# Kernel optimization log

Hardware: AMD Instinct MI355X
Metric: run time of the kernel (lower is better)

## Reference

```python
import jax, jax.numpy as jnp
import numpy as np
from jax import lax

NEG_INF = -jnp.inf

def _conv_same(x, w, b):
    # x: [B,C,H,W], w: [O,C,5,5], padding=2 (SAME for k=5)
    y = lax.conv_general_dilated(x, w, (1, 1), [(2, 2), (2, 2)],
                                 dimension_numbers=('NCHW', 'OIHW', 'NCHW'))
    return y + b[None, :, None, None]

def _maxpool3(x):
    # kernel=3, stride=3, VALID: 28x28 -> 9x9
    return lax.reduce_window(x, -jnp.inf, lax.max, (1, 1, 3, 3), (1, 1, 3, 3), 'VALID')

def _trunk(x, w1, b1, w2, b2):
    # x: [B,1,28,28] -> [B, 16*9*9]
    h = jax.nn.relu(_conv_same(x, w1, b1))
    h = jax.nn.relu(_conv_same(h, w2, b2))
    h = _maxpool3(h)
    return h.reshape(h.shape[0], -1)

def _iterator(state, c_w1, c_b1, c_w2, c_b2, c_wl, c_bl):
    # state: [B,28,28]
    B = state.shape[0]
    xd = state[:, None]                                   # [B,1,28,28]
    feat = _trunk(xd, c_w1, c_b1, c_w2, c_b2)             # [B,1296]
    w = jnp.tanh(feat @ c_wl + c_bl).reshape(B, 1, 13, 13)  # per-sample kernels [O=B,I=1,13,13]
    xp = jnp.pad(xd, ((0, 0), (0, 0), (6, 6), (6, 6)), constant_values=-1.0)  # [B,1,40,40]
    xg = xp.reshape(1, B, 40, 40)
    yg = lax.conv_general_dilated(xg, w, (1, 1), 'VALID',
                                  feature_group_count=B,
                                  dimension_numbers=('NCHW', 'OIHW', 'NCHW'))  # [1,B,28,28]
    return yg.reshape(B, 28, 28)

def setup_inputs() -> dict:
    key = jax.random.key(0)
    ks = jax.random.split(key, 13)
    s = 0.05
    B = 1024
    inp = {
        'x': jax.random.normal(ks[0], (B, 28, 28), jnp.float32),
        # determine_n params
        'n_w1': jax.random.normal(ks[1], (8, 1, 5, 5), jnp.float32) * s,
        'n_b1': jnp.zeros((8,), jnp.float32),
        'n_w2': jax.random.normal(ks[2], (16, 8, 5, 5), jnp.float32) * s,
        'n_b2': jnp.zeros((16,), jnp.float32),
        'n_wl': jax.random.normal(ks[3], (16 * 9 * 9, 10), jnp.float32) * s,
        'n_bl': jnp.zeros((10,), jnp.float32),
        # determine_conv params
        'c_w1': jax.random.normal(ks[4], (8, 1, 5, 5), jnp.float32) * s,
        'c_b1': jnp.zeros((8,), jnp.float32),
        'c_w2': jax.random.normal(ks[5], (16, 8, 5, 5), jnp.float32) * s,
        'c_b2': jnp.zeros((16,), jnp.float32),
        'c_wl': jax.random.normal(ks[6], (16 * 9 * 9, 13 * 13), jnp.float32) * s,
        'c_bl': jnp.zeros((13 * 13,), jnp.float32),
    }
    return inp

def reference(x, n_w1, n_b1, n_w2, n_b2, n_wl, n_bl,
              c_w1, c_b1, c_w2, c_b2, c_wl, c_bl):
    B = x.shape[0]
    xd = x.reshape(B, 1, 28, 28)
    # determine_n: soft natural number over {0..9}
    num = jnp.tanh(_trunk(xd, n_w1, n_b1, n_w2, n_b2) @ n_wl + n_bl)  # [B,10]
    # TmIter: weighted sum of iterates r_0..r_9, r_{k+1} = iterator(r_k)
    r = x
    out = num[:, 0, None, None] * r
    for k in range(1, 10):  # fixed 9-step unroll (num encodes naturals 0..9)
        r = _iterator(r, c_w1, c_b1, c_w2, c_b2, c_wl, c_bl)
        out = out + num[:, k, None, None] * r
    return out.reshape(-1, 28, 28)
```

## Files before the change

### kernel.cpp

```cpp
#include <hip/hip_runtime.h>
#include <math.h>

#define RP40S 44
#define H1W   31

struct SharedBufs {
    float rp40[2][40*RP40S];
    float h1p[8*28*H1W];
    float pbuf[1296];
    float wker[169];
    float num_s[10];
    int   next;
};

template<int OUT>
__device__ __forceinline__ void fc_tanh(const float* __restrict__ Wg,
                                        const float* __restrict__ bg,
                                        const float* __restrict__ p,
                                        float* __restrict__ dst, int tid)
{
    if (tid < OUT) {
        float a[8];
        #pragma unroll
        for (int u = 0; u < 8; ++u) a[u] = 0.f;
        #pragma unroll 4
        for (int i0 = 0; i0 < 1296; i0 += 8) {
            const float4 p0 = *(const float4*)&p[i0];
            const float4 p1 = *(const float4*)&p[i0+4];
            a[0] = fmaf(p0.x, Wg[(i0+0)*OUT + tid], a[0]);
            a[1] = fmaf(p0.y, Wg[(i0+1)*OUT + tid], a[1]);
            a[2] = fmaf(p0.z, Wg[(i0+2)*OUT + tid], a[2]);
            a[3] = fmaf(p0.w, Wg[(i0+3)*OUT + tid], a[3]);
            a[4] = fmaf(p1.x, Wg[(i0+4)*OUT + tid], a[4]);
            a[5] = fmaf(p1.y, Wg[(i0+5)*OUT + tid], a[5]);
            a[6] = fmaf(p1.z, Wg[(i0+6)*OUT + tid], a[6]);
            a[7] = fmaf(p1.w, Wg[(i0+7)*OUT + tid], a[7]);
        }
        float s = ((a[0]+a[1])+(a[2]+a[3])) + ((a[4]+a[5])+(a[6]+a[7])) + bg[tid];
        dst[tid] = tanhf(s);
    }
}

#define C2_LOADROW(dst, YY) {                                                  \
    int rr_ = crow0 + (YY); rr_ = rr_ < 2 ? 2 : (rr_ > 29 ? 29 : rr_);         \
    const float* hp_ = plane + (rr_ - 2)*H1W;                                  \
    _Pragma("unroll") for (int j = 0; j < 13; ++j) dst[j] = hp_[j]; }

#define C2_FMAROW(src, YY)                                                     \
    if ((unsigned)(crow0 + (YY) - 2) <= 27u) {                                 \
      _Pragma("unroll") for (int t = 0; t < 3; ++t) {                          \
        const int ky_ = (YY) - t;                                              \
        if (ky_ >= 0 && ky_ <= 4) {                                            \
          _Pragma("unroll") for (int kx = 0; kx < 5; ++kx) {                   \
            const float w_ = wreg[ky_*5+kx];                                   \
            _Pragma("unroll") for (int u = 0; u < 9; ++u)                      \
              acc[t*9+u] = fmaf(w_, src[u+kx], acc[t*9+u]); } } } }

__device__ __forceinline__ void trunk_pass(SharedBufs& sb,
                                           const float* __restrict__ rpc,
                                           int tid,
                                           const float* __restrict__ w1g,
                                           const float* __restrict__ b1g,
                                           const float* __restrict__ w2g,
                                           const float* __restrict__ b2g)
{
    if (tid < 224) {
        const int c = tid & 7;
        const int y = tid >> 3;
        float wreg[25];
        #pragma unroll
        for (int t = 0; t < 25; ++t) wreg[t] = w1g[c*25 + t];
        float csR[5];
        float S_all = 0.f, SR = 0.f;
        #pragma unroll
        for (int kx = 0; kx < 5; ++kx) {
            float a = wreg[kx] + wreg[5+kx] + wreg[10+kx] + wreg[15+kx] + wreg[20+kx];
            float ex = 0.f;
            if (y == 0)       ex = wreg[kx] + wreg[5+kx];
            else if (y == 1)  ex = wreg[kx];
            if (y == 26)      ex += wreg[20+kx];
            else if (y == 27) ex += wreg[15+kx] + wreg[20+kx];
            csR[kx] = a - ex;
            S_all += a; SR += csR[kx];
        }
        const float corrI = S_all - SR;
        const float bias  = b1g[c];
        float acc[28];
        #pragma unroll
        for (int x = 0; x < 28; ++x) acc[x] = bias + corrI;
        acc[0]  += csR[0] + csR[1];
        acc[1]  += csR[0];
        acc[26] += csR[4];
        acc[27] += csR[3] + csR[4];
        #pragma unroll
        for (int ky = 0; ky < 5; ++ky) {
            const float4* rr = (const float4*)&rpc[(y+4+ky)*RP40S + 4];
            float rv[32];
            #pragma unroll
            for (int q = 0; q < 8; ++q) {
                float4 t = rr[q];
                rv[q*4+0]=t.x; rv[q*4+1]=t.y; rv[q*4+2]=t.z; rv[q*4+3]=t.w;
            }
            #pragma unroll
            for (int kx = 0; kx < 5; ++kx) {
                const float w = wreg[ky*5+kx];
                #pragma unroll
                for (int x = 0; x < 28; ++x) acc[x] = fmaf(w, rv[x+kx], acc[x]);
            }
        }
        float* hp = &sb.h1p[(c*28 + y)*H1W + 2];
        #pragma unroll
        for (int x = 0; x < 28; ++x) hp[x] = fmaxf(acc[x], 0.f);
    }
    __syncthreads();

    if (tid < 240) {
        const int c    = tid / 15;
        const int rem  = tid % 15;
        const int pyg  = rem / 3;
        const int pxg  = rem % 3;
        const int col0 = pxg * 9;
        const float bias = b2g[c];
        #pragma unroll 1
        for (int h = 0; h < 2; ++h) {
            const int py = pyg*2 + h;
            if (py >= 9) break;
            const int crow0 = py * 3;
            float acc[27];
            #pragma unroll
            for (int i = 0; i < 27; ++i) acc[i] = bias;
            for (int ic = 0; ic < 8; ++ic) {
                float wreg[25];
                const float* wsrc = &w2g[(c*8+ic)*25];
                #pragma unroll
                for (int t = 0; t < 25; ++t) wreg[t] = wsrc[t];
                const float* plane = &sb.h1p[ic*28*H1W + col0];
                float ra[13], rb[13];
                C2_LOADROW(ra, 0)
                C2_LOADROW(rb, 1)  C2_FMAROW(ra, 0)
                C2_LOADROW(ra, 2)  C2_FMAROW(rb, 1)
                C2_LOADROW(rb, 3)  C2_FMAROW(ra, 2)
                C2_LOADROW(ra, 4)  C2_FMAROW(rb, 3)
                C2_LOADROW(rb, 5)  C2_FMAROW(ra, 4)
                C2_LOADROW(ra, 6)  C2_FMAROW(rb, 5)
                                   C2_FMAROW(ra, 6)
            }
            #pragma unroll
            for (int pxi = 0; pxi < 3; ++pxi) {
                float m = acc[pxi*3];
                #pragma unroll
                for (int dy = 0; dy < 3; ++dy)
                    #pragma unroll
                    for (int dx = 0; dx < 3; ++dx)
                        m = fmaxf(m, acc[dy*9 + pxi*3 + dx]);
                sb.pbuf[c*81 + py*9 + pxg*3 + pxi] = fmaxf(m, 0.f);
            }
        }
    }
    __syncthreads();
}

__device__ __forceinline__ void depthwise13_regs(SharedBufs& sb,
                                                 const float* __restrict__ rpc,
                                                 int y, int x0,
                                                 float& a0, float& a1,
                                                 float& a2, float& a3)
{
    a0=0.f; a1=0.f; a2=0.f; a3=0.f;
    #pragma unroll 1
    for (int ky = 0; ky < 13; ++ky) {
        const float4* rr = (const float4*)&rpc[(y+ky)*RP40S + x0];
        float rv[16];
        #pragma unroll
        for (int q = 0; q < 4; ++q) {
            float4 t = rr[q];
            rv[q*4+0]=t.x; rv[q*4+1]=t.y; rv[q*4+2]=t.z; rv[q*4+3]=t.w;
        }
        const float* wr = &sb.wker[ky*13];
        #pragma unroll
        for (int kx = 0; kx < 13; ++kx) {
            const float w = wr[kx];
            a0 = fmaf(w, rv[kx+0], a0);
            a1 = fmaf(w, rv[kx+1], a1);
            a2 = fmaf(w, rv[kx+2], a2);
            a3 = fmaf(w, rv[kx+3], a3);
        }
    }
}

__global__ __launch_bounds__(256) __attribute__((amdgpu_num_vgpr(168)))
void modeld_fused(const float* __restrict__ x,
                  const float* __restrict__ n_w1, const float* __restrict__ n_b1,
                  const float* __restrict__ n_w2, const float* __restrict__ n_b2,
                  const float* __restrict__ n_wl, const float* __restrict__ n_bl,
                  const float* __restrict__ c_w1, const float* __restrict__ c_b1,
                  const float* __restrict__ c_w2, const float* __restrict__ c_b2,
                  const float* __restrict__ c_wl, const float* __restrict__ c_bl,
                  float* __restrict__ out,
                  int* __restrict__ counter, int B)
{
    __shared__ SharedBufs sb;
    const int tid = threadIdx.x;
    const int dy  = tid / 7;
    const int dx0 = (tid % 7) * 4;

    for (int i = tid; i < 2*40*RP40S; i += 256) sb.rp40[0][i] = -1.f;
    for (int i = tid; i < 8*28*H1W;   i += 256) sb.h1p[i]  = 0.f;

    while (true) {
        if (tid == 0) sb.next = atomicAdd(counter, 1);
        __syncthreads();
        const int b = sb.next;
        if (b >= B) break;

        float cur[4] = {0.f, 0.f, 0.f, 0.f};
        if (tid < 196) {
            const float4 t = *(const float4*)&x[b*784 + dy*28 + dx0];
            cur[0]=t.x; cur[1]=t.y; cur[2]=t.z; cur[3]=t.w;
            float* rp = &sb.rp40[0][(dy+6)*RP40S + dx0 + 6];
            rp[0]=t.x; rp[1]=t.y; rp[2]=t.z; rp[3]=t.w;
        }
        __syncthreads();

        trunk_pass(sb, sb.rp40[0], tid, n_w1, n_b1, n_w2, n_b2);
        fc_tanh<10>(n_wl, n_bl, sb.pbuf, sb.num_s, tid);
        __syncthreads();

        float o[4];
        {
            const float n0 = sb.num_s[0];
            #pragma unroll
            for (int q = 0; q < 4; ++q) o[q] = n0 * cur[q];
        }

        int curbuf = 0;
        for (int k = 1; k <= 9; ++k) {
            const float* rpc = sb.rp40[curbuf];
            float*       rpn = sb.rp40[curbuf ^ 1];
            trunk_pass(sb, rpc, tid, c_w1, c_b1, c_w2, c_b2);
            fc_tanh<169>(c_wl, c_bl, sb.pbuf, sb.wker, tid);
            __syncthreads();
            if (tid < 196) {
                float a0, a1, a2, a3;
                depthwise13_regs(sb, rpc, dy, dx0, a0, a1, a2, a3);
                const float nk = sb.num_s[k];
                o[0] = fmaf(nk, a0, o[0]);
                o[1] = fmaf(nk, a1, o[1]);
                o[2] = fmaf(nk, a2, o[2]);
                o[3] = fmaf(nk, a3, o[3]);
                float* rp = &rpn[(dy+6)*RP40S + dx0 + 6];
                rp[0]=a0; rp[1]=a1; rp[2]=a2; rp[3]=a3;
            }
            __syncthreads();
            curbuf ^= 1;
        }

        if (tid < 196)
            *(float4*)&out[b*784 + dy*28 + dx0] = make_float4(o[0], o[1], o[2], o[3]);
    }
}

extern "C" void kernel_launch(void* const* d_in, const int* in_sizes, int n_in,
                              void* d_out, int out_size, void* d_ws, size_t ws_size,
                              hipStream_t stream)
{
    const float* x    = (const float*)d_in[0];
    const float* n_w1 = (const float*)d_in[1];
    const float* n_b1 = (const float*)d_in[2];
    const float* n_w2 = (const float*)d_in[3];
    const float* n_b2 = (const float*)d_in[4];
    const float* n_wl = (const float*)d_in[5];
    const float* n_bl = (const float*)d_in[6];
    const float* c_w1 = (const float*)d_in[7];
    const float* c_b1 = (const float*)d_in[8];
    const float* c_w2 = (const float*)d_in[9];
    const float* c_b2 = (const float*)d_in[10];
    const float* c_wl = (const float*)d_in[11];
    const float* c_bl = (const float*)d_in[12];
    float* out = (float*)d_out;

    const int B = in_sizes[0] / 784;
    hipMemsetAsync(d_ws, 0, sizeof(int), stream);
    const int grid = B < 768 ? B : 768;
    hipLaunchKernelGGL(modeld_fused, dim3(grid), dim3(256), 0, stream,
                       x, n_w1, n_b1, n_w2, n_b2, n_wl, n_bl,
                       c_w1, c_b1, c_w2, c_b2, c_wl, c_bl, out,
                       (int*)d_ws, B);
}
```

Before: 1.335 ms.

## Hoist conv1 border corrections, pad depthwise kernel rows, unroll FC deeper

Computes the conv1 bias and border-correction terms once per thread at kernel start instead of on every trunk pass, passing them in as scalars. Pads the 13x13 dynamic kernel rows to stride 16 so the depthwise loop can read weights with float4 LDS loads. Raises the FC loop unroll from 4 to 8. Keeping ten extra live scalars across the persistent loop adds register pressure under the fixed 168-VGPR cap, which could cause spills.

New measurement: 1.302 ms, median of 2. 1.03x faster.

```diff
diff --git a/kernel.cpp b/kernel.cpp
--- a/kernel.cpp
+++ b/kernel.cpp
@@ -8,12 +8,12 @@
     float rp40[2][40*RP40S];
     float h1p[8*28*H1W];
     float pbuf[1296];
-    float wker[169];
+    float wker[13*16];
     float num_s[10];
     int   next;
 };
 
-template<int OUT>
+template<int OUT, bool PAD>
 __device__ __forceinline__ void fc_tanh(const float* __restrict__ Wg,
                                         const float* __restrict__ bg,
                                         const float* __restrict__ p,
@@ -23,7 +23,7 @@
         float a[8];
         #pragma unroll
         for (int u = 0; u < 8; ++u) a[u] = 0.f;
-        #pragma unroll 4
+        #pragma unroll 8
         for (int i0 = 0; i0 < 1296; i0 += 8) {
             const float4 p0 = *(const float4*)&p[i0];
             const float4 p1 = *(const float4*)&p[i0+4];
@@ -37,8 +37,37 @@
             a[7] = fmaf(p1.w, Wg[(i0+7)*OUT + tid], a[7]);
         }
         float s = ((a[0]+a[1])+(a[2]+a[3])) + ((a[4]+a[5])+(a[6]+a[7])) + bg[tid];
-        dst[tid] = tanhf(s);
-    }
+        dst[PAD ? (tid/13)*16 + (tid%13) : tid] = tanhf(s);
+    }
+}
+
+__device__ __forceinline__ void conv1_corr(const float* __restrict__ w1g,
+                                           const float* __restrict__ b1g,
+                                           int c, int y,
+                                           float& base, float& e0, float& e1,
+                                           float& e26, float& e27)
+{
+    float wreg[25];
+    #pragma unroll
+    for (int t = 0; t < 25; ++t) wreg[t] = w1g[c*25 + t];
+    float csR[5];
+    float S_all = 0.f, SR = 0.f;
+    #pragma unroll
+    for (int kx = 0; kx < 5; ++kx) {
+        float a = wreg[kx] + wreg[5+kx] + wreg[10+kx] + wreg[15+kx] + wreg[20+kx];
+        float ex = 0.f;
+        if (y == 0)       ex = wreg[kx] + wreg[5+kx];
+        else if (y == 1)  ex = wreg[kx];
+        if (y == 26)      ex += wreg[20+kx];
+        else if (y == 27) ex += wreg[15+kx] + wreg[20+kx];
+        csR[kx] = a - ex;
+        S_all += a; SR += csR[kx];
+    }
+    base = b1g[c] + (S_all - SR);
+    e0  = csR[0] + csR[1];
+    e1  = csR[0];
+    e26 = csR[4];
+    e27 = csR[3] + csR[4];
 }
 
 #define C2_LOADROW(dst, YY) {                                                  \
@@ -60,9 +89,10 @@
                                            const float* __restrict__ rpc,
                                            int tid,
                                            const float* __restrict__ w1g,
-                                           const float* __restrict__ b1g,
                                            const float* __restrict__ w2g,
-                                           const float* __restrict__ b2g)
+                                           const float* __restrict__ b2g,
+                                           float base, float e0, float e1,
+                                           float e26, float e27)
 {
     if (tid < 224) {
         const int c = tid & 7;
@@ -70,28 +100,13 @@
         float wreg[25];
         #pragma unroll
         for (int t = 0; t < 25; ++t) wreg[t] = w1g[c*25 + t];
-        float csR[5];
-        float S_all = 0.f, SR = 0.f;
-        #pragma unroll
-        for (int kx = 0; kx < 5; ++kx) {
-            float a = wreg[kx] + wreg[5+kx] + wreg[10+kx] + wreg[15+kx] + wreg[20+kx];
-            float ex = 0.f;
-            if (y == 0)       ex = wreg[kx] + wreg[5+kx];
-            else if (y == 1)  ex = wreg[kx];
-            if (y == 26)      ex += wreg[20+kx];
-            else if (y == 27) ex += wreg[15+kx] + wreg[20+kx];
-            csR[kx] = a - ex;
-            S_all += a; SR += csR[kx];
-        }
-        const float corrI = S_all - SR;
-        const float bias  = b1g[c];
         float acc[28];
         #pragma unroll
-        for (int x = 0; x < 28; ++x) acc[x] = bias + corrI;
-        acc[0]  += csR[0] + csR[1];
-        acc[1]  += csR[0];
-        acc[26] += csR[4];
-        acc[27] += csR[3] + csR[4];
+        for (int x = 0; x < 28; ++x) acc[x] = base;
+        acc[0]  += e0;
+        acc[1]  += e1;
+        acc[26] += e26;
+        acc[27] += e27;
         #pragma unroll
         for (int ky = 0; ky < 5; ++ky) {
             const float4* rr = (const float4*)&rpc[(y+4+ky)*RP40S + 4];
@@ -176,10 +191,16 @@
             float4 t = rr[q];
             rv[q*4+0]=t.x; rv[q*4+1]=t.y; rv[q*4+2]=t.z; rv[q*4+3]=t.w;
         }
-        const float* wr = &sb.wker[ky*13];
+        const float4* wq = (const float4*)&sb.wker[ky*16];
+        float wv[16];
+        #pragma unroll
+        for (int q = 0; q < 4; ++q) {
+            float4 t = wq[q];
+            wv[q*4+0]=t.x; wv[q*4+1]=t.y; wv[q*4+2]=t.z; wv[q*4+3]=t.w;
+        }
         #pragma unroll
         for (int kx = 0; kx < 13; ++kx) {
-            const float w = wr[kx];
+            const float w = wv[kx];
             a0 = fmaf(w, rv[kx+0], a0);
             a1 = fmaf(w, rv[kx+1], a1);
             a2 = fmaf(w, rv[kx+2], a2);
@@ -204,6 +225,13 @@
     const int dy  = tid / 7;
     const int dx0 = (tid % 7) * 4;
 
+    float nb=0.f, ne0=0.f, ne1=0.f, ne26=0.f, ne27=0.f;
+    float cb=0.f, ce0=0.f, ce1=0.f, ce26=0.f, ce27=0.f;
+    if (tid < 224) {
+        conv1_corr(n_w1, n_b1, tid & 7, tid >> 3, nb, ne0, ne1, ne26, ne27);
+        conv1_corr(c_w1, c_b1, tid & 7, tid >> 3, cb, ce0, ce1, ce26, ce27);
+    }
+
     for (int i = tid; i < 2*40*RP40S; i += 256) sb.rp40[0][i] = -1.f;
     for (int i = tid; i < 8*28*H1W;   i += 256) sb.h1p[i]  = 0.f;
 
@@ -222,8 +250,8 @@
         }
         __syncthreads();
 
-        trunk_pass(sb, sb.rp40[0], tid, n_w1, n_b1, n_w2, n_b2);
-        fc_tanh<10>(n_wl, n_bl, sb.pbuf, sb.num_s, tid);
+        trunk_pass(sb, sb.rp40[0], tid, n_w1, n_w2, n_b2, nb, ne0, ne1, ne26, ne27);
+        fc_tanh<10, false>(n_wl, n_bl, sb.pbuf, sb.num_s, tid);
         __syncthreads();
 
         float o[4];
@@ -237,8 +265,8 @@
         for (int k = 1; k <= 9; ++k) {
             const float* rpc = sb.rp40[curbuf];
             float*       rpn = sb.rp40[curbuf ^ 1];
-            trunk_pass(sb, rpc, tid, c_w1, c_b1, c_w2, c_b2);
-            fc_tanh<169>(c_wl, c_bl, sb.pbuf, sb.wker, tid);
+            trunk_pass(sb, rpc, tid, c_w1, c_w2, c_b2, cb, ce0, ce1, ce26, ce27);
+            fc_tanh<169, true>(c_wl, c_bl, sb.pbuf, sb.wker, tid);
             __syncthreads();
             if (tid < 196) {
                 float a0, a1, a2, a3;
```
